# Kernel optimization log

Measured on AMD Instinct MI355X. Metric: run time of the kernel, lower is better.

The kernel has to match this reference:

```python
import jax, jax.numpy as jnp
import numpy as np

N_EMB = 100000
DIM = 64
BATCH = 16384
HIST = 200


def setup_inputs() -> dict:
    key = jax.random.key(0)
    k_idx, k_w = jax.random.split(key)
    indices = jax.random.randint(k_idx, (BATCH, HIST), 0, N_EMB, dtype=jnp.int64 if jax.config.jax_enable_x64 else jnp.int32)
    # torch.nn.Linear(n_embeddings, dim, bias=False) weight has shape [dim, n_embeddings]
    W = jax.random.normal(k_w, (DIM, N_EMB), dtype=jnp.float32)
    return {"indices": indices, "W": W}


def reference(indices, W):
    # Original: onehot(indices) [B,H,N] @ W.T [N,D]  ==  gather of W.T rows.
    # Same math expressed as a direct lookup (no N x N eye materialized).
    table = W.T  # [n_embeddings, dim]
    return table[indices]  # [BATCH, HIST, dim]
```

## Files before the change

### kernel.cpp

```cpp
#include <hip/hip_runtime.h>

#define N_EMB 100000
#define DIM   64

typedef float    f32x4 __attribute__((ext_vector_type(4)));
typedef _Float16 f16x4 __attribute__((ext_vector_type(4)));

__global__ void transpose_w_h(const float* __restrict__ W,
                              _Float16* __restrict__ table,
                              int n_emb) {
    __shared__ float tile[64][65];
    const int n0   = blockIdx.x * 64;
    const int t    = threadIdx.x;
    const int lane = t & 63;
    const int grp  = t >> 6;

    #pragma unroll
    for (int i = 0; i < 16; ++i) {
        const int d = grp * 16 + i;
        const int n = n0 + lane;
        tile[d][lane] = (n < n_emb) ? W[(long long)d * N_EMB + n] : 0.0f;
    }
    __syncthreads();

    #pragma unroll
    for (int i = 0; i < 16; ++i) {
        const int n = n0 + grp * 16 + i;
        if (n < n_emb)
            table[(long long)n * DIM + lane] = (_Float16)tile[lane][grp * 16 + i];
    }
}

__global__ void __launch_bounds__(256) gather_h4(
        const int* __restrict__ idx,
        const f16x4* __restrict__ tableh,
        f32x4* __restrict__ out4,
        long long total_f4) {
    const long long stride = (long long)gridDim.x * blockDim.x;
    for (long long g = (long long)blockIdx.x * blockDim.x + threadIdx.x;
         g < total_f4; g += stride) {
        const int id = idx[g >> 4];
        const int e  = (int)(g & 15);
        const f16x4 h = tableh[(long long)id * 16 + e];
        const f32x4 v = __builtin_convertvector(h, f32x4);
        __builtin_nontemporal_store(v, out4 + g);
    }
}

__global__ void gather_direct(const int* __restrict__ idx,
                              const float* __restrict__ W,
                              float* __restrict__ out,
                              long long total) {
    const long long stride = (long long)gridDim.x * blockDim.x;
    for (long long g = (long long)blockIdx.x * blockDim.x + threadIdx.x;
         g < total; g += stride) {
        out[g] = W[(long long)(g & 63) * N_EMB + idx[g >> 6]];
    }
}

extern "C" void kernel_launch(void* const* d_in, const int* in_sizes, int n_in,
                              void* d_out, int out_size, void* d_ws, size_t ws_size,
                              hipStream_t stream) {
    const int*   idx = (const int*)d_in[0];
    const float* W   = (const float*)d_in[1];
    float*       out = (float*)d_out;

    const long long total     = (long long)out_size;
    const size_t    tbl_bytes = (size_t)N_EMB * DIM * sizeof(_Float16);

    if (ws_size >= tbl_bytes) {
        _Float16* table = (_Float16*)d_ws;

        transpose_w_h<<<(N_EMB + 63) / 64, 256, 0, stream>>>(W, table, N_EMB);

        const long long total_f4 = total / 4;
        gather_h4<<<2048, 256, 0, stream>>>(idx, (const f16x4*)table,
                                            (f32x4*)out, total_f4);
    } else {
        gather_direct<<<2048, 256, 0, stream>>>(idx, W, out, total);
    }
}
```

Before: 185.6 us.

## Bucket gather indices by table slice in shared memory for cache locality

Each block loads 1600 indices, bins them into four table-range slices with shared-memory atomics, then gathers slice by slice so concurrent reads concentrate on a smaller portion of the fp16 table. This aims to improve L2 hit rate on the random table reads. It adds atomics, a barrier, shared-memory usage that limits occupancy, and less sequential output writes, with an overflow path for full buckets.

```diff
diff --git a/kernel.cpp b/kernel.cpp
--- a/kernel.cpp
+++ b/kernel.cpp
@@ -2,6 +2,11 @@
 
 #define N_EMB 100000
 #define DIM   64
+
+#define NSLICE       4
+#define SLICE_ROWS   ((N_EMB + NSLICE - 1) / NSLICE)
+#define ROWS_PER_BLK 1600
+#define CAPL         560
 
 typedef float    f32x4 __attribute__((ext_vector_type(4)));
 typedef _Float16 f16x4 __attribute__((ext_vector_type(4)));
@@ -31,19 +36,47 @@
     }
 }
 
-__global__ void __launch_bounds__(256) gather_h4(
-        const int* __restrict__ idx,
+__global__ void __launch_bounds__(256) gather_sliced(
+        const int* __restrict__ idx, long long n_idx,
         const f16x4* __restrict__ tableh,
-        f32x4* __restrict__ out4,
-        long long total_f4) {
-    const long long stride = (long long)gridDim.x * blockDim.x;
-    for (long long g = (long long)blockIdx.x * blockDim.x + threadIdx.x;
-         g < total_f4; g += stride) {
-        const int id = idx[g >> 4];
-        const int e  = (int)(g & 15);
-        const f16x4 h = tableh[(long long)id * 16 + e];
-        const f32x4 v = __builtin_convertvector(h, f32x4);
-        __builtin_nontemporal_store(v, out4 + g);
+        f32x4* __restrict__ out4) {
+    __shared__ int  cnt[NSLICE];
+    __shared__ int2 list[NSLICE][CAPL];
+
+    const int t = threadIdx.x;
+    const long long base = (long long)blockIdx.x * ROWS_PER_BLK;
+
+    if (t < NSLICE) cnt[t] = 0;
+    __syncthreads();
+
+    for (int i = t; i < ROWS_PER_BLK; i += 256) {
+        const long long r = base + i;
+        if (r < n_idx) {
+            const int id  = idx[r];
+            const int s   = id / SLICE_ROWS;
+            const int pos = atomicAdd(&cnt[s], 1);
+            if (pos < CAPL) {
+                list[s][pos] = make_int2(id, i);
+            } else {
+                #pragma unroll
+                for (int q = 0; q < 16; ++q)
+                    out4[r * 16 + q] =
+                        __builtin_convertvector(tableh[(long long)id * 16 + q], f32x4);
+            }
+        }
+    }
+    __syncthreads();
+
+    const int g = t >> 4;
+    const int e = t & 15;
+    for (int p = 0; p < NSLICE; ++p) {
+        const int np = min(cnt[p], CAPL);
+        for (int i = g; i < np; i += 16) {
+            const int2  a = list[p][i];
+            const f16x4 h = tableh[(long long)a.x * 16 + e];
+            const f32x4 v = __builtin_convertvector(h, f32x4);
+            __builtin_nontemporal_store(v, out4 + (base + a.y) * 16 + e);
+        }
     }
 }
 
@@ -65,6 +98,7 @@
     const float* W   = (const float*)d_in[1];
     float*       out = (float*)d_out;
 
+    const long long n_idx     = (long long)in_sizes[0];
     const long long total     = (long long)out_size;
     const size_t    tbl_bytes = (size_t)N_EMB * DIM * sizeof(_Float16);
 
@@ -73,9 +107,10 @@
 
         transpose_w_h<<<(N_EMB + 63) / 64, 256, 0, stream>>>(W, table, N_EMB);
 
-        const long long total_f4 = total / 4;
-        gather_h4<<<2048, 256, 0, stream>>>(idx, (const f16x4*)table,
-                                            (f32x4*)out, total_f4);
+        const int gblocks = (int)((n_idx + ROWS_PER_BLK - 1) / ROWS_PER_BLK);
+        gather_sliced<<<gblocks, 256, 0, stream>>>(idx, n_idx,
+                                                   (const f16x4*)table,
+                                                   (f32x4*)out);
     } else {
         gather_direct<<<2048, 256, 0, stream>>>(idx, W, out, total);
     }
```

Measured after the change: 188.3 us. About the same (+1.4%).
